# Performance work log

Measured on AMD Instinct MI355X. Metric: run time of the kernel, lower is better.

The kernel has to match this reference:

```python
import jax, jax.numpy as jnp
import numpy as np
from jax import lax

B, C, H, W = 8192, 256, 5, 5
G = 8
SE_HID = 64        # max(8, 256 // 4)
GN_EPS = 1e-5
MM_EPS = 1e-8


def group_norm(x, gamma, beta):
    # x: [B, C, H, W]; normalize per (group, H, W)
    b = x.shape[0]
    xg = x.reshape(b, G, C // G, H, W)
    mean = xg.mean(axis=(2, 3, 4), keepdims=True)
    var = xg.var(axis=(2, 3, 4), keepdims=True)
    xg = (xg - mean) * lax.rsqrt(var + GN_EPS)
    xn = xg.reshape(b, C, H, W)
    return xn * gamma[None, :, None, None] + beta[None, :, None, None]


def setup_inputs() -> dict:
    key = jax.random.key(0)
    ks = jax.random.split(key, 10)
    x = jax.random.normal(ks[0], (B, C, H, W), dtype=jnp.float32)
    pair_mask = (jax.random.uniform(ks[1], (B, 1, H, W)) < 0.8).astype(jnp.float32)
    s1 = 1.0 / np.sqrt(C)
    W1 = jax.random.normal(ks[2], (C, C), dtype=jnp.float32) * s1          # 1x1 conv
    W2 = jax.random.normal(ks[3], (C, C, 3, 3), dtype=jnp.float32) * (s1 / 3.0)
    g1 = jnp.ones((C,), jnp.float32); b1 = jnp.zeros((C,), jnp.float32)
    g2 = jnp.ones((C,), jnp.float32); b2 = jnp.zeros((C,), jnp.float32)
    fc1_w = jax.random.normal(ks[4], (SE_HID, C), dtype=jnp.float32) * s1
    fc1_b = jnp.zeros((SE_HID,), jnp.float32)
    fc2_w = jax.random.normal(ks[5], (C, SE_HID), dtype=jnp.float32) / np.sqrt(SE_HID)
    fc2_b = jnp.zeros((C,), jnp.float32)
    return {"x": x, "pair_mask": pair_mask, "W1": W1, "g1": g1, "b1": b1,
            "W2": W2, "g2": g2, "b2": b2,
            "fc1_w": fc1_w, "fc1_b": fc1_b, "fc2_w": fc2_w, "fc2_b": fc2_b}


def reference(x, pair_mask, W1, g1, b1, W2, g2, b2, fc1_w, fc1_b, fc2_w, fc2_b):
    residual = x
    # conv1: 1x1, no bias -> channel mixing
    out = jnp.einsum('bchw,oc->bohw', x, W1)
    out = jax.nn.gelu(group_norm(out, g1, b1), approximate=False)
    # conv2: 3x3, padding=1, no bias
    out = lax.conv_general_dilated(out, W2, window_strides=(1, 1),
                                   padding=((1, 1), (1, 1)),
                                   dimension_numbers=('NCHW', 'OIHW', 'NCHW'))
    out = jax.nn.gelu(group_norm(out, g2, b2), approximate=False)
    out = out + residual
    # masked SE
    denom = jnp.maximum(pair_mask.sum(axis=(-1, -2)), MM_EPS)   # [B,1]
    pooled = (out * pair_mask).sum(axis=(-1, -2)) / denom       # [B,C]
    h = jax.nn.gelu(pooled @ fc1_w.T + fc1_b, approximate=False)
    gate = jax.nn.sigmoid(h @ fc2_w.T + fc2_b)                  # [B,C]
    out = out * gate[:, :, None, None] * pair_mask              # SE mask
    out = out * pair_mask                                       # final mask
    return out, gate
```

## Files before the change

### kernel.cpp

```cpp
#include <hip/hip_runtime.h>
#include <math.h>


typedef short v8s  __attribute__((ext_vector_type(8)));
typedef short v4s  __attribute__((ext_vector_type(4)));
typedef float v16f __attribute__((ext_vector_type(16)));
typedef float v4f  __attribute__((ext_vector_type(4)));

#define NTHREADS 512
#define NB 2
#define CP 264
#define CPB 528
#define YROWS 49
#define YSB (YROWS*CPB)

#define Y_BYTES   (NB*YSB)
#define GB_OFF    (Y_BYTES)
#define MASK_OFF  (GB_OFF + 1024*4)
#define POOL_OFF  (MASK_OFF + NB*32*4)
#define H_OFF     (POOL_OFF + NB*256*4)
#define GATE_OFF  (H_OFF + NB*64*4)
#define INVD_OFF  (GATE_OFF + NB*256*4)
#define SMEM_BYTES (INVD_OFF + 64)

__device__ __forceinline__ unsigned short f2bf(float f){
  unsigned u = __float_as_uint(f);
  u = u + 0x7fffu + ((u >> 16) & 1u);
  return (unsigned short)(u >> 16);
}
__device__ __forceinline__ float gelu_f(float v){
  float z  = fabsf(v) * 0.70710678118654752f;
  float t  = __builtin_amdgcn_rcpf(fmaf(0.3275911f, z, 1.0f));
  float e  = __builtin_amdgcn_exp2f(-z*z*1.4426950408889634f);
  float p  = fmaf(1.061405429f, t, -1.453152027f);
  p = fmaf(p, t, 1.421413741f);
  p = fmaf(p, t, -0.284496736f);
  p = fmaf(p, t, 0.254829592f);
  float er = fmaf(-p*t, e, 1.0f);
  er = __builtin_copysignf(er, v);
  return 0.5f*v*(1.0f + er);
}

__global__ void prep_kernel(const float* __restrict__ W1, const float* __restrict__ W2,
                            const float* __restrict__ fc1w, const float* __restrict__ fc2w,
                            unsigned short* __restrict__ w1p, unsigned short* __restrict__ w2p,
                            float* __restrict__ fc1t, float* __restrict__ fc2t)
{
  int t = blockIdx.x*blockDim.x + threadIdx.x;
  int stride = gridDim.x*blockDim.x;
  for (int i=t; i<16*256*16; i+=stride){
    int s=i>>12, o=(i>>4)&255, kk=i&15;
    w1p[i] = f2bf(W1[o*256 + s*16 + kk]);
  }
  for (int i=t; i<144*256*16; i+=stride){
    int s=i>>12, o=(i>>4)&255, kk=i&15;
    int tap=s>>4, cb=s&15;
    w2p[i] = f2bf(W2[o*2304 + (cb*16+kk)*9 + tap]);
  }
  for (int i=t; i<256*64; i+=stride){ int c=i>>6, h=i&63; fc1t[i]=fc1w[h*256+c]; }
  for (int i=t; i<64*256; i+=stride){ int k=i>>8, c=i&255; fc2t[i]=fc2w[c*64+k]; }
}

__global__ __launch_bounds__(NTHREADS, 4) void lrb_main(
    const float* __restrict__ xg, const float* __restrict__ maskg,
    const float* __restrict__ g1, const float* __restrict__ b1,
    const float* __restrict__ g2, const float* __restrict__ b2,
    const unsigned short* __restrict__ w1p, const unsigned short* __restrict__ w2p,
    const float* __restrict__ fc1t, const float* __restrict__ fc1b,
    const float* __restrict__ fc2t, const float* __restrict__ fc2b,
    float* __restrict__ outg, float* __restrict__ gateg)
{
  extern __shared__ char smem[];
  float* OUTF = (float*)smem;
  float* GB   = (float*)(smem + GB_OFF);
  float* MS   = (float*)(smem + MASK_OFF);
  float* POOL = (float*)(smem + POOL_OFF);
  float* HS   = (float*)(smem + H_OFF);
  float* GT   = (float*)(smem + GATE_OFF);
  float* INVD = (float*)(smem + INVD_OFF);

  const int tid  = threadIdx.x;
  const int lane = tid & 63;
  const int wid  = tid >> 6;
  const int p    = lane & 31;
  const int half = lane >> 5;
  const int hx   = half << 4;
  const bool pv  = (p < 25);
  const int b0   = blockIdx.x * NB;

  {
    int4 z4; z4.x=z4.y=z4.z=z4.w=0;
    for (int i = tid; i < NB*24*33; i += NTHREADS){
      int nbb = i / 792;
      int rem = i - nbb*792;
      int rr  = 25 + rem/33, cc = rem - (rem/33)*33;
      *(int4*)(smem + nbb*YSB + rr*CPB + cc*16) = z4;
    }
    if (tid < 256){
      GB[tid]=g1[tid]; GB[256+tid]=b1[tid]; GB[512+tid]=g2[tid]; GB[768+tid]=b2[tid];
    }
    if (tid >= 256 && tid < 256 + NB*32){
      int t2 = tid - 256;
      int nbb = t2>>5, pp = t2&31;
      MS[t2] = (pp < 25) ? maskg[(size_t)(b0+nbb)*25 + pp] : 0.f;
    }
  }

  const int pr = p/5, ps = p - 5*(p/5);
  const int pbase = pv ? (7*pr + ps) : 0;
  const int row1  = p;
  const int kx1   = ((row1>>3)&3)<<4;
  const size_t aoff = (size_t)((wid*32 + p)*16 + half*8) * 2;
  const char* w1c = (const char*)w1p;
  const char* w2c = (const char*)w2p;

  v8s A1r[4], B1r[2][2];
  #pragma unroll
  for (int s0=0; s0<4; ++s0) A1r[s0] = *(const v8s*)(w1c + s0*8192 + aoff);

  __syncthreads();

  if (tid < NB){
    float s=0.f;
    #pragma unroll
    for (int pp=0;pp<25;++pp) s += MS[tid*32+pp];
    INVD[tid] = __builtin_amdgcn_rcpf(fmaxf(s, 1e-8f));
  }

  for (int i = tid; i < NB*25*32; i += NTHREADS){
    int nbb = i / 800;
    int rem = i - nbb*800;
    int pp  = rem >> 5;
    int c8  = rem & 31;
    const float* src = xg + ((size_t)(b0+nbb)*256 + c8*8)*25 + pp;
    v8s pk;
    #pragma unroll
    for (int k=0;k<8;++k) pk[k] = (short)f2bf(src[k*25]);
    int off = (c8<<4) ^ (((pp>>3)&3)<<4);
    *(v8s*)(smem + nbb*YSB + pp*CPB + off) = pk;
  }
  __syncthreads();

  v16f acc1[2];
  #pragma unroll
  for (int j=0;j<16;++j){ acc1[0][j]=0.f; acc1[1][j]=0.f; }

  #pragma unroll
  for (int s0=0; s0<2; ++s0)
    #pragma unroll
    for (int nt=0; nt<2; ++nt)
      B1r[s0][nt] = *(const v8s*)(smem + nt*YSB + row1*CPB + (((s0<<5)|hx)^kx1));

  #pragma unroll
  for (int s=0; s<16; ++s){
    acc1[0] = __builtin_amdgcn_mfma_f32_32x32x16_bf16(A1r[s&3], B1r[s&1][0], acc1[0], 0,0,0);
    acc1[1] = __builtin_amdgcn_mfma_f32_32x32x16_bf16(A1r[s&3], B1r[s&1][1], acc1[1], 0,0,0);
    if (s+4 < 16) A1r[s&3] = *(const v8s*)(w1c + (s+4)*8192 + aoff);
    if (s+2 < 16){
      #pragma unroll
      for (int nt=0; nt<2; ++nt)
        B1r[s&1][nt] = *(const v8s*)(smem + nt*YSB + row1*CPB + ((((s+2)<<5)|hx)^kx1));
    }
  }

  {
    float s_[2], q_[2];
    #pragma unroll
    for (int nt=0;nt<2;++nt){
      float a=0.f, b=0.f;
      #pragma unroll
      for (int j=0;j<16;++j){ float v = acc1[nt][j]; a += v; b += v*v; }
      s_[nt]=a; q_[nt]=b;
    }
    #pragma unroll
    for (int off=1; off<64; off<<=1){
      #pragma unroll
      for (int nt=0;nt<2;++nt){
        s_[nt] += __shfl_xor(s_[nt], off, 64);
        q_[nt] += __shfl_xor(q_[nt], off, 64);
      }
    }
    __syncthreads();

    const int grow = pbase + 8;
    const int kxg  = ((grow>>3)&3)<<4;
    #pragma unroll
    for (int nt=0;nt<2;++nt){
      float mu = s_[nt]*(1.f/800.f);
      float vr = q_[nt]*(1.f/800.f) - mu*mu;
      float rstd = rsqrtf(vr + 1e-5f);
      if (pv){
        #pragma unroll
        for (int q=0;q<4;++q){
          int ch0 = wid*32 + 8*q + 4*half;
          v4s pk;
          #pragma unroll
          for (int i2=0;i2<4;++i2){
            int ch = ch0 + i2;
            float f = (acc1[nt][4*q+i2]-mu)*rstd*GB[ch]+GB[256+ch];
            pk[i2] = (short)f2bf(gelu_f(f));
          }
          *(v4s*)(smem + nt*YSB + grow*CPB + (((wid<<6)+(q<<4)+(half<<3)) ^ kxg)) = pk;
        }
      }
    }
  }
  {
    int4 z4; z4.x=z4.y=z4.z=z4.w=0;
    for (int i = tid; i < NB*12*33; i += NTHREADS){
      int nbb = i / 396;
      int rem = i - nbb*396;
      int rr  = rem/33, cc = rem - (rem/33)*33;
      int row = rr < 8 ? rr : (rr < 10 ? rr + 5 : rr + 10);
      *(int4*)(smem + nbb*YSB + row*CPB + cc*16) = z4;
    }
  }

  v8s A2r[6], B2r[2][2];
  #pragma unroll
  for (int s0=0; s0<6; ++s0) A2r[s0] = *(const v8s*)(w2c + s0*8192 + aoff);
  __syncthreads();

  v16f acc2[2];
  #pragma unroll
  for (int j=0;j<16;++j){ acc2[0][j]=0.f; acc2[1][j]=0.f; }

  {
    constexpr int OFF7[9] = {0,1,2,7,8,9,14,15,16};
    #pragma unroll
    for (int s0=0; s0<2; ++s0){
      int row2 = pv ? (pbase + OFF7[0]) : (p-24);
      int off  = row2*CPB + (((s0<<5)|hx) ^ (((row2>>3)&3)<<4));
      B2r[s0][0] = *(const v8s*)(smem + off);
      B2r[s0][1] = *(const v8s*)(smem + YSB + off);
    }
    #pragma unroll
    for (int s=0; s<144; ++s){
      acc2[0] = __builtin_amdgcn_mfma_f32_32x32x16_bf16(A2r[s%6], B2r[s&1][0], acc2[0], 0,0,0);
      acc2[1] = __builtin_amdgcn_mfma_f32_32x32x16_bf16(A2r[s%6], B2r[s&1][1], acc2[1], 0,0,0);
      if (s+6 < 144) A2r[s%6] = *(const v8s*)(w2c + (s+6)*8192 + aoff);
      if (s+2 < 144){
        int s2 = s+2;
        int tap = s2>>4, cb = s2&15;
        int row2 = pv ? (pbase + OFF7[tap]) : (p-24);
        int off  = row2*CPB + (((cb<<5)|hx) ^ (((row2>>3)&3)<<4));
        B2r[s&1][0] = *(const v8s*)(smem + off);
        B2r[s&1][1] = *(const v8s*)(smem + YSB + off);
      }
    }
  }

  {
    float s_[2], q_[2];
    #pragma unroll
    for (int nt=0;nt<2;++nt){
      float a=0.f, b=0.f;
      #pragma unroll
      for (int j=0;j<16;++j){ float v = acc2[nt][j]; a += v; b += v*v; }
      s_[nt]=a; q_[nt]=b;
    }
    #pragma unroll
    for (int off=1; off<64; off<<=1){
      #pragma unroll
      for (int nt=0;nt<2;++nt){
        s_[nt] += __shfl_xor(s_[nt], off, 64);
        q_[nt] += __shfl_xor(q_[nt], off, 64);
      }
    }
    __syncthreads();

    float psum[2][16];
    #pragma unroll
    for (int nt=0;nt<2;++nt){
      float mu = s_[nt]*(1.f/800.f);
      float vr = q_[nt]*(1.f/800.f) - mu*mu;
      float rstd = rsqrtf(vr + 1e-5f);
      float mk = pv ? MS[nt*32+p] : 0.f;
      const float* xr = xg + ((size_t)(b0+nt)*256 + wid*32)*25 + p;
      #pragma unroll
      for (int j=0;j<16;++j){
        int crow = (j&3) + 8*(j>>2) + 4*half;
        int ch   = wid*32 + crow;
        float f = (acc2[nt][j]-mu)*rstd*GB[512+ch]+GB[768+ch];
        f = gelu_f(f);
        if (pv){
          f += xr[crow*25];
          OUTF[nt*6400 + ch*25 + p] = f;
        }
        psum[nt][j] = f*mk;
      }
    }
    #pragma unroll
    for (int off=1; off<32; off<<=1)
      #pragma unroll
      for (int nt=0;nt<2;++nt)
        #pragma unroll
        for (int j=0;j<16;++j)
          psum[nt][j] += __shfl_xor(psum[nt][j], off, 64);
    if ((lane&31)==0){
      #pragma unroll
      for (int nt=0;nt<2;++nt)
        #pragma unroll
        for (int j=0;j<16;++j)
          POOL[nt*256 + wid*32 + (j&3)+8*(j>>2)+4*half] = psum[nt][j];
    }
  }
  __syncthreads();

  {
    int nbb  = tid >> 8;
    int hid  = (tid >> 2) & 63;
    int part = tid & 3;
    const float* pl = POOL + nbb*256 + part*64;
    const float* wp = fc1t + part*64*64 + hid;
    float dot = 0.f;
    #pragma unroll 8
    for (int c=0;c<64;++c) dot += wp[c*64]*pl[c];
    dot += __shfl_xor(dot, 1, 64);
    dot += __shfl_xor(dot, 2, 64);
    if (part == 0)
      HS[nbb*64+hid] = gelu_f(fmaf(INVD[nbb], dot, fc1b[hid]));
  }
  __syncthreads();
  {
    int ch = tid & 255, nbb = tid >> 8;
    const float* hp = HS + nbb*64;
    float dot = 0.f;
    #pragma unroll 8
    for (int k=0;k<64;++k) dot += fc2t[k*256+ch]*hp[k];
    dot += fc2b[ch];
    float gv = __builtin_amdgcn_rcpf(1.0f + __builtin_amdgcn_exp2f(-dot*1.4426950408889634f));
    GT[nbb*256+ch] = gv;
    gateg[(size_t)(b0+nbb)*256+ch] = gv;
  }
  __syncthreads();

  for (int i = tid; i < NB*1600; i += NTHREADS){
    int nbb = i / 1600;
    int r4  = i - nbb*1600;
    int e0  = r4*4;
    v4f o4 = *(const v4f*)(OUTF + nbb*6400 + e0);
    #pragma unroll
    for (int k=0;k<4;++k){
      int e = e0+k;
      int ch = e/25;
      int pp = e - ch*25;
      o4[k] = o4[k] * GT[nbb*256+ch] * MS[nbb*32+pp];
    }
    *(v4f*)(outg + (size_t)(b0+nbb)*6400 + e0) = o4;
  }
}

extern "C" void kernel_launch(void* const* d_in, const int* in_sizes, int n_in,
                              void* d_out, int out_size, void* d_ws, size_t ws_size,
                              hipStream_t stream)
{
  const float* xg   = (const float*)d_in[0];
  const float* pm   = (const float*)d_in[1];
  const float* W1   = (const float*)d_in[2];
  const float* g1   = (const float*)d_in[3];
  const float* b1   = (const float*)d_in[4];
  const float* W2   = (const float*)d_in[5];
  const float* g2   = (const float*)d_in[6];
  const float* b2   = (const float*)d_in[7];
  const float* fc1w = (const float*)d_in[8];
  const float* fc1b = (const float*)d_in[9];
  const float* fc2w = (const float*)d_in[10];
  const float* fc2b = (const float*)d_in[11];

  float* outg  = (float*)d_out;
  float* gateg = outg + (size_t)8192*256*25;

  unsigned short* w1p = (unsigned short*)d_ws;
  unsigned short* w2p = w1p + 16*256*16;
  float* fc1t = (float*)(w2p + 144*256*16);
  float* fc2t = fc1t + 256*64;

  prep_kernel<<<dim3(512), dim3(256), 0, stream>>>(W1, W2, fc1w, fc2w, w1p, w2p, fc1t, fc2t);

  hipFuncSetAttribute(reinterpret_cast<const void*>(lrb_main),
                      hipFuncAttributeMaxDynamicSharedMemorySize, (int)SMEM_BYTES);
  lrb_main<<<dim3(4096), dim3(NTHREADS), SMEM_BYTES, stream>>>(
      xg, pm, g1, b1, g2, b2, w1p, w2p, fc1t, fc1b, fc2t, fc2b, outg, gateg);
}
```

Baseline: 606.4 us.

## Split conv2 K across wave pairs with 64-row tiles and LDS reduction

Conv2 is repartitioned so each wave computes 64 output channels (two A tiles) over half of the K dimension, issuing four MFMAs per step. This reuses each B fragment across two A tiles and halves the per-wave step count. Partial sums are then combined through an LDS exchange with extra barriers. The XOR swizzle is replaced by a wider padded row stride, and the conv1 prefetch depth is changed. The trade-off is more accumulator registers and extra reduction synchronisation.

```diff
diff --git a/kernel.cpp b/kernel.cpp
--- a/kernel.cpp
+++ b/kernel.cpp
@@ -9,18 +9,17 @@
 
 #define NTHREADS 512
 #define NB 2
-#define CP 264
-#define CPB 528
+#define CPB 560
 #define YROWS 49
 #define YSB (YROWS*CPB)
 
-#define Y_BYTES   (NB*YSB)
-#define GB_OFF    (Y_BYTES)
-#define MASK_OFF  (GB_OFF + 1024*4)
-#define POOL_OFF  (MASK_OFF + NB*32*4)
-#define H_OFF     (POOL_OFF + NB*256*4)
-#define GATE_OFF  (H_OFF + NB*64*4)
-#define INVD_OFF  (GATE_OFF + NB*256*4)
+#define Y_BYTES  (NB*YSB)
+#define GB_OFF   (Y_BYTES)
+#define MASK_OFF (GB_OFF + 4096)
+#define POOL_OFF (MASK_OFF + 256)
+#define H_OFF    (POOL_OFF + 2048)
+#define GATE_OFF (H_OFF + 512)
+#define INVD_OFF (GATE_OFF + 2048)
 #define SMEM_BYTES (INVD_OFF + 64)
 
 __device__ __forceinline__ unsigned short f2bf(float f){
@@ -39,6 +38,21 @@
   float er = fmaf(-p*t, e, 1.0f);
   er = __builtin_copysignf(er, v);
   return 0.5f*v*(1.0f + er);
+}
+
+__device__ __forceinline__ void v16store(char* dst, const v16f &v){
+  #pragma unroll
+  for (int q=0;q<4;++q){
+    v4f t; t[0]=v[4*q]; t[1]=v[4*q+1]; t[2]=v[4*q+2]; t[3]=v[4*q+3];
+    *(v4f*)(dst + q*1024) = t;
+  }
+}
+__device__ __forceinline__ void v16addload(const char* src, v16f &v){
+  #pragma unroll
+  for (int q=0;q<4;++q){
+    v4f t = *(const v4f*)(src + q*1024);
+    v[4*q]+=t[0]; v[4*q+1]+=t[1]; v[4*q+2]+=t[2]; v[4*q+3]+=t[3];
+  }
 }
 
 __global__ void prep_kernel(const float* __restrict__ W1, const float* __restrict__ W2,
@@ -82,6 +96,8 @@
   const int tid  = threadIdx.x;
   const int lane = tid & 63;
   const int wid  = tid >> 6;
+  const int mp   = wid >> 1;
+  const int kh   = wid & 1;
   const int p    = lane & 31;
   const int half = lane >> 5;
   const int hx   = half << 4;
@@ -90,10 +106,10 @@
 
   {
     int4 z4; z4.x=z4.y=z4.z=z4.w=0;
-    for (int i = tid; i < NB*24*33; i += NTHREADS){
-      int nbb = i / 792;
-      int rem = i - nbb*792;
-      int rr  = 25 + rem/33, cc = rem - (rem/33)*33;
+    for (int i = tid; i < NB*24*35; i += NTHREADS){
+      int nbb = i / 840;
+      int rem = i - nbb*840;
+      int rr  = 25 + rem/35, cc = rem - (rem/35)*35;
       *(int4*)(smem + nbb*YSB + rr*CPB + cc*16) = z4;
     }
     if (tid < 256){
@@ -108,24 +124,18 @@
 
   const int pr = p/5, ps = p - 5*(p/5);
   const int pbase = pv ? (7*pr + ps) : 0;
-  const int row1  = p;
-  const int kx1   = ((row1>>3)&3)<<4;
-  const size_t aoff = (size_t)((wid*32 + p)*16 + half*8) * 2;
+  const int pbCPB = pbase*CPB;
+  const int zCPB  = (p-24)*CPB;
+  const int bcol  = hx + kh*256;
   const char* w1c = (const char*)w1p;
   const char* w2c = (const char*)w2p;
-
-  v8s A1r[4], B1r[2][2];
-  #pragma unroll
-  for (int s0=0; s0<4; ++s0) A1r[s0] = *(const v8s*)(w1c + s0*8192 + aoff);
-
-  __syncthreads();
-
-  if (tid < NB){
-    float s=0.f;
-    #pragma unroll
-    for (int pp=0;pp<25;++pp) s += MS[tid*32+pp];
-    INVD[tid] = __builtin_amdgcn_rcpf(fmaxf(s, 1e-8f));
-  }
+  const int aoff1 = (wid*32 + p)*32 + hx;
+  const char* w2base = w2c + kh*65536 + mp*2048 + p*32 + hx;
+  const char* Yb1[2] = { smem + p*CPB + hx, smem + YSB + p*CPB + hx };
+
+  v8s A1[3], B1[3][2];
+  #pragma unroll
+  for (int s0=0; s0<3; ++s0) A1[s0] = *(const v8s*)(w1c + s0*8192 + aoff1);
 
   for (int i = tid; i < NB*25*32; i += NTHREADS){
     int nbb = i / 800;
@@ -136,173 +146,189 @@
     v8s pk;
     #pragma unroll
     for (int k=0;k<8;++k) pk[k] = (short)f2bf(src[k*25]);
-    int off = (c8<<4) ^ (((pp>>3)&3)<<4);
-    *(v8s*)(smem + nbb*YSB + pp*CPB + off) = pk;
-  }
-  __syncthreads();
-
-  v16f acc1[2];
-  #pragma unroll
-  for (int j=0;j<16;++j){ acc1[0][j]=0.f; acc1[1][j]=0.f; }
-
-  #pragma unroll
-  for (int s0=0; s0<2; ++s0)
-    #pragma unroll
-    for (int nt=0; nt<2; ++nt)
-      B1r[s0][nt] = *(const v8s*)(smem + nt*YSB + row1*CPB + (((s0<<5)|hx)^kx1));
-
+    *(v8s*)(smem + nbb*YSB + pp*CPB + c8*16) = pk;
+  }
+  __syncthreads();
+
+  if (tid < NB){
+    float s=0.f;
+    #pragma unroll
+    for (int pp=0;pp<25;++pp) s += MS[tid*32+pp];
+    INVD[tid] = __builtin_amdgcn_rcpf(fmaxf(s, 1e-8f));
+  }
+
+  v16f acc1_0, acc1_1;
+  #pragma unroll
+  for (int j=0;j<16;++j){ acc1_0[j]=0.f; acc1_1[j]=0.f; }
+  #pragma unroll
+  for (int s0=0; s0<3; ++s0){
+    B1[s0][0] = *(const v8s*)(Yb1[0] + s0*32);
+    B1[s0][1] = *(const v8s*)(Yb1[1] + s0*32);
+  }
   #pragma unroll
   for (int s=0; s<16; ++s){
-    acc1[0] = __builtin_amdgcn_mfma_f32_32x32x16_bf16(A1r[s&3], B1r[s&1][0], acc1[0], 0,0,0);
-    acc1[1] = __builtin_amdgcn_mfma_f32_32x32x16_bf16(A1r[s&3], B1r[s&1][1], acc1[1], 0,0,0);
-    if (s+4 < 16) A1r[s&3] = *(const v8s*)(w1c + (s+4)*8192 + aoff);
-    if (s+2 < 16){
+    acc1_0 = __builtin_amdgcn_mfma_f32_32x32x16_bf16(A1[s%3], B1[s%3][0], acc1_0, 0,0,0);
+    acc1_1 = __builtin_amdgcn_mfma_f32_32x32x16_bf16(A1[s%3], B1[s%3][1], acc1_1, 0,0,0);
+    if (s+3 < 16){
+      A1[s%3] = *(const v8s*)(w1c + (s+3)*8192 + aoff1);
+      B1[s%3][0] = *(const v8s*)(Yb1[0] + (s+3)*32);
+      B1[s%3][1] = *(const v8s*)(Yb1[1] + (s+3)*32);
+    }
+  }
+
+  {
+    float s0a=0.f,q0a=0.f,s1a=0.f,q1a=0.f;
+    #pragma unroll
+    for (int j=0;j<16;++j){
+      float v0 = acc1_0[j], v1 = acc1_1[j];
+      s0a+=v0; q0a+=v0*v0; s1a+=v1; q1a+=v1*v1;
+    }
+    #pragma unroll
+    for (int off=1; off<64; off<<=1){
+      s0a += __shfl_xor(s0a, off, 64); q0a += __shfl_xor(q0a, off, 64);
+      s1a += __shfl_xor(s1a, off, 64); q1a += __shfl_xor(q1a, off, 64);
+    }
+    __syncthreads();
+
+    const int grow = pbase + 8;
+    float mu0 = s0a*(1.f/800.f), mu1 = s1a*(1.f/800.f);
+    float rstd0 = rsqrtf(q0a*(1.f/800.f) - mu0*mu0 + 1e-5f);
+    float rstd1 = rsqrtf(q1a*(1.f/800.f) - mu1*mu1 + 1e-5f);
+    if (pv){
       #pragma unroll
-      for (int nt=0; nt<2; ++nt)
-        B1r[s&1][nt] = *(const v8s*)(smem + nt*YSB + row1*CPB + ((((s+2)<<5)|hx)^kx1));
-    }
-  }
-
-  {
-    float s_[2], q_[2];
-    #pragma unroll
-    for (int nt=0;nt<2;++nt){
-      float a=0.f, b=0.f;
-      #pragma unroll
-      for (int j=0;j<16;++j){ float v = acc1[nt][j]; a += v; b += v*v; }
-      s_[nt]=a; q_[nt]=b;
-    }
-    #pragma unroll
-    for (int off=1; off<64; off<<=1){
-      #pragma unroll
-      for (int nt=0;nt<2;++nt){
-        s_[nt] += __shfl_xor(s_[nt], off, 64);
-        q_[nt] += __shfl_xor(q_[nt], off, 64);
-      }
-    }
-    __syncthreads();
-
-    const int grow = pbase + 8;
-    const int kxg  = ((grow>>3)&3)<<4;
-    #pragma unroll
-    for (int nt=0;nt<2;++nt){
-      float mu = s_[nt]*(1.f/800.f);
-      float vr = q_[nt]*(1.f/800.f) - mu*mu;
-      float rstd = rsqrtf(vr + 1e-5f);
-      if (pv){
+      for (int nt=0; nt<2; ++nt){
+        float mu = nt ? mu1 : mu0, rstd = nt ? rstd1 : rstd0;
+        char* dst = smem + nt*YSB + grow*CPB + wid*64 + half*8;
         #pragma unroll
         for (int q=0;q<4;++q){
-          int ch0 = wid*32 + 8*q + 4*half;
           v4s pk;
           #pragma unroll
           for (int i2=0;i2<4;++i2){
-            int ch = ch0 + i2;
-            float f = (acc1[nt][4*q+i2]-mu)*rstd*GB[ch]+GB[256+ch];
+            int ch = wid*32 + q*8 + half*4 + i2;
+            float v = nt ? acc1_1[4*q+i2] : acc1_0[4*q+i2];
+            float f = (v-mu)*rstd*GB[ch]+GB[256+ch];
             pk[i2] = (short)f2bf(gelu_f(f));
           }
-          *(v4s*)(smem + nt*YSB + grow*CPB + (((wid<<6)+(q<<4)+(half<<3)) ^ kxg)) = pk;
+          *(v4s*)(dst + q*16) = pk;
         }
       }
     }
   }
   {
     int4 z4; z4.x=z4.y=z4.z=z4.w=0;
-    for (int i = tid; i < NB*12*33; i += NTHREADS){
-      int nbb = i / 396;
-      int rem = i - nbb*396;
-      int rr  = rem/33, cc = rem - (rem/33)*33;
+    for (int i = tid; i < NB*12*35; i += NTHREADS){
+      int nbb = i / 420;
+      int rem = i - nbb*420;
+      int rr  = rem/35, cc = rem - (rem/35)*35;
       int row = rr < 8 ? rr : (rr < 10 ? rr + 5 : rr + 10);
       *(int4*)(smem + nbb*YSB + row*CPB + cc*16) = z4;
     }
   }
 
-  v8s A2r[6], B2r[2][2];
-  #pragma unroll
-  for (int s0=0; s0<6; ++s0) A2r[s0] = *(const v8s*)(w2c + s0*8192 + aoff);
-  __syncthreads();
-
-  v16f acc2[2];
-  #pragma unroll
-  for (int j=0;j<16;++j){ acc2[0][j]=0.f; acc2[1][j]=0.f; }
+  v8s A2[3][2], B2[3][2];
+  #pragma unroll
+  for (int s0=0; s0<3; ++s0){
+    A2[s0][0] = *(const v8s*)(w2base + (s0>>3)*131072 + (s0&7)*8192);
+    A2[s0][1] = *(const v8s*)(w2base + (s0>>3)*131072 + (s0&7)*8192 + 1024);
+  }
+  __syncthreads();
+
+  v16f acc2_00, acc2_01, acc2_10, acc2_11;
+  #pragma unroll
+  for (int j=0;j<16;++j){ acc2_00[j]=0.f; acc2_01[j]=0.f; acc2_10[j]=0.f; acc2_11[j]=0.f; }
 
   {
     constexpr int OFF7[9] = {0,1,2,7,8,9,14,15,16};
     #pragma unroll
-    for (int s0=0; s0<2; ++s0){
-      int row2 = pv ? (pbase + OFF7[0]) : (p-24);
-      int off  = row2*CPB + (((s0<<5)|hx) ^ (((row2>>3)&3)<<4));
-      B2r[s0][0] = *(const v8s*)(smem + off);
-      B2r[s0][1] = *(const v8s*)(smem + YSB + off);
-    }
-    #pragma unroll
-    for (int s=0; s<144; ++s){
-      acc2[0] = __builtin_amdgcn_mfma_f32_32x32x16_bf16(A2r[s%6], B2r[s&1][0], acc2[0], 0,0,0);
-      acc2[1] = __builtin_amdgcn_mfma_f32_32x32x16_bf16(A2r[s%6], B2r[s&1][1], acc2[1], 0,0,0);
-      if (s+6 < 144) A2r[s%6] = *(const v8s*)(w2c + (s+6)*8192 + aoff);
-      if (s+2 < 144){
-        int s2 = s+2;
-        int tap = s2>>4, cb = s2&15;
-        int row2 = pv ? (pbase + OFF7[tap]) : (p-24);
-        int off  = row2*CPB + (((cb<<5)|hx) ^ (((row2>>3)&3)<<4));
-        B2r[s&1][0] = *(const v8s*)(smem + off);
-        B2r[s&1][1] = *(const v8s*)(smem + YSB + off);
-      }
-    }
-  }
-
-  {
-    float s_[2], q_[2];
-    #pragma unroll
-    for (int nt=0;nt<2;++nt){
-      float a=0.f, b=0.f;
+    for (int s0=0; s0<3; ++s0){
+      int ro = pv ? (pbCPB + OFF7[0]*CPB) : zCPB;
+      B2[s0][0] = *(const v8s*)(smem + ro + bcol + (s0&7)*32);
+      B2[s0][1] = *(const v8s*)(smem + YSB + ro + bcol + (s0&7)*32);
+    }
+    #pragma unroll
+    for (int s=0; s<72; ++s){
+      acc2_00 = __builtin_amdgcn_mfma_f32_32x32x16_bf16(A2[s%3][0], B2[s%3][0], acc2_00, 0,0,0);
+      acc2_01 = __builtin_amdgcn_mfma_f32_32x32x16_bf16(A2[s%3][0], B2[s%3][1], acc2_01, 0,0,0);
+      acc2_10 = __builtin_amdgcn_mfma_f32_32x32x16_bf16(A2[s%3][1], B2[s%3][0], acc2_10, 0,0,0);
+      acc2_11 = __builtin_amdgcn_mfma_f32_32x32x16_bf16(A2[s%3][1], B2[s%3][1], acc2_11, 0,0,0);
+      if (s+3 < 72){
+        int s3 = s+3;
+        A2[s%3][0] = *(const v8s*)(w2base + (s3>>3)*131072 + (s3&7)*8192);
+        A2[s%3][1] = *(const v8s*)(w2base + (s3>>3)*131072 + (s3&7)*8192 + 1024);
+        int ro = pv ? (pbCPB + OFF7[s3>>3]*CPB) : zCPB;
+        B2[s%3][0] = *(const v8s*)(smem + ro + bcol + (s3&7)*32);
+        B2[s%3][1] = *(const v8s*)(smem + YSB + ro + bcol + (s3&7)*32);
+      }
+    }
+  }
+  __syncthreads();
+
+  {
+    char* EXw = smem + (kh^1)*16384 + mp*4096 + (lane<<4);
+    const char* EXr = smem + kh*16384 + mp*4096 + (lane<<4);
+    if (kh==0) v16store(EXw, acc2_01); else v16store(EXw, acc2_00);
+    __syncthreads();
+    if (kh==0) v16addload(EXr, acc2_00); else v16addload(EXr, acc2_01);
+    __syncthreads();
+    if (kh==0) v16store(EXw, acc2_11); else v16store(EXw, acc2_10);
+    __syncthreads();
+    if (kh==0) v16addload(EXr, acc2_10); else v16addload(EXr, acc2_11);
+  }
+  v16f F0 = (kh==0) ? acc2_00 : acc2_01;
+  v16f F1 = (kh==0) ? acc2_10 : acc2_11;
+
+  {
+    float s0a=0.f,q0a=0.f,s1a=0.f,q1a=0.f;
+    #pragma unroll
+    for (int j=0;j<16;++j){
+      float v0=F0[j], v1=F1[j];
+      s0a+=v0; q0a+=v0*v0; s1a+=v1; q1a+=v1*v1;
+    }
+    #pragma unroll
+    for (int off=1; off<64; off<<=1){
+      s0a += __shfl_xor(s0a, off, 64); q0a += __shfl_xor(q0a, off, 64);
+      s1a += __shfl_xor(s1a, off, 64); q1a += __shfl_xor(q1a, off, 64);
+    }
+    __syncthreads();
+
+    float mu0 = s0a*(1.f/800.f), mu1 = s1a*(1.f/800.f);
+    float rstd0 = rsqrtf(q0a*(1.f/800.f) - mu0*mu0 + 1e-5f);
+    float rstd1 = rsqrtf(q1a*(1.f/800.f) - mu1*mu1 + 1e-5f);
+    float mk = pv ? MS[kh*32+p] : 0.f;
+    const float* xr = xg + ((size_t)(b0+kh)*256 + mp*64)*25 + p;
+    float ps0[16], ps1[16];
+    #pragma unroll
+    for (int j=0;j<16;++j){
+      int crow = (j&3) + 8*(j>>2) + 4*half;
+      {
+        int ch = mp*64 + crow;
+        float f = (F0[j]-mu0)*rstd0*GB[512+ch]+GB[768+ch];
+        f = gelu_f(f);
+        if (pv){ f += xr[crow*25]; OUTF[kh*6400 + ch*25 + p] = f; }
+        ps0[j] = f*mk;
+      }
+      {
+        int ch = mp*64 + 32 + crow;
+        float f = (F1[j]-mu1)*rstd1*GB[512+ch]+GB[768+ch];
+        f = gelu_f(f);
+        if (pv){ f += xr[(32+crow)*25]; OUTF[kh*6400 + ch*25 + p] = f; }
+        ps1[j] = f*mk;
+      }
+    }
+    #pragma unroll
+    for (int off=1; off<32; off<<=1)
       #pragma unroll
-      for (int j=0;j<16;++j){ float v = acc2[nt][j]; a += v; b += v*v; }
-      s_[nt]=a; q_[nt]=b;
-    }
-    #pragma unroll
-    for (int off=1; off<64; off<<=1){
-      #pragma unroll
-      for (int nt=0;nt<2;++nt){
-        s_[nt] += __shfl_xor(s_[nt], off, 64);
-        q_[nt] += __shfl_xor(q_[nt], off, 64);
-      }
-    }
-    __syncthreads();
-
-    float psum[2][16];
-    #pragma unroll
-    for (int nt=0;nt<2;++nt){
-      float mu = s_[nt]*(1.f/800.f);
-      float vr = q_[nt]*(1.f/800.f) - mu*mu;
-      float rstd = rsqrtf(vr + 1e-5f);
-      float mk = pv ? MS[nt*32+p] : 0.f;
-      const float* xr = xg + ((size_t)(b0+nt)*256 + wid*32)*25 + p;
+      for (int j=0;j<16;++j){
+        ps0[j] += __shfl_xor(ps0[j], off, 64);
+        ps1[j] += __shfl_xor(ps1[j], off, 64);
+      }
+    if ((lane&31)==0){
       #pragma unroll
       for (int j=0;j<16;++j){
         int crow = (j&3) + 8*(j>>2) + 4*half;
-        int ch   = wid*32 + crow;
-        float f = (acc2[nt][j]-mu)*rstd*GB[512+ch]+GB[768+ch];
-        f = gelu_f(f);
-        if (pv){
-          f += xr[crow*25];
-          OUTF[nt*6400 + ch*25 + p] = f;
-        }
-        psum[nt][j] = f*mk;
-      }
-    }
-    #pragma unroll
-    for (int off=1; off<32; off<<=1)
-      #pragma unroll
-      for (int nt=0;nt<2;++nt)
-        #pragma unroll
-        for (int j=0;j<16;++j)
-          psum[nt][j] += __shfl_xor(psum[nt][j], off, 64);
-    if ((lane&31)==0){
-      #pragma unroll
-      for (int nt=0;nt<2;++nt)
-        #pragma unroll
-        for (int j=0;j<16;++j)
-          POOL[nt*256 + wid*32 + (j&3)+8*(j>>2)+4*half] = psum[nt][j];
+        POOL[kh*256 + mp*64 + crow]      = ps0[j];
+        POOL[kh*256 + mp*64 + 32 + crow] = ps1[j];
+      }
     }
   }
   __syncthreads();
```

Result: no change. 615.7 us (+1.5%).
